# Performance work log

Measured on AMD Instinct MI355X. Metric: run time of the kernel, lower is better.

## Reference

```python
import jax, jax.numpy as jnp
import numpy as np

C_IN = 512
NUM_HEADS = 8
D_K = 64
D_V = 64


def setup_inputs() -> dict:
    key = jax.random.key(0)
    ks = jax.random.split(key, 6)
    scale = 1.0 / np.sqrt(C_IN)
    return {
        "x": jax.random.normal(ks[0], (8, C_IN, 32, 32), dtype=jnp.float32),
        "Wq": jax.random.normal(ks[1], (C_IN, NUM_HEADS * D_K), dtype=jnp.float32) * scale,
        "bq": jnp.zeros((NUM_HEADS * D_K,), dtype=jnp.float32),
        "Wk": jax.random.normal(ks[2], (C_IN, NUM_HEADS * D_K), dtype=jnp.float32) * scale,
        "bk": jnp.zeros((NUM_HEADS * D_K,), dtype=jnp.float32),
        "Wv": jax.random.normal(ks[3], (C_IN, NUM_HEADS * D_V), dtype=jnp.float32) * scale,
        "bv": jnp.zeros((NUM_HEADS * D_V,), dtype=jnp.float32),
        "Wo": jax.random.normal(ks[4], (NUM_HEADS * D_V, C_IN), dtype=jnp.float32) * scale,
        "bo": jnp.zeros((C_IN,), dtype=jnp.float32),
        "num_heads": NUM_HEADS,
    }


def reference(x, Wq, bq, Wk, bk, Wv, bv, Wo, bo, num_heads):
    B, C, H, W = x.shape
    S = H * W
    xs = x.reshape(B, C, S).transpose(0, 2, 1)  # [B, S, C]

    def split_heads(t):  # [B, S, nh*d] -> [B, nh, S, d]
        return t.reshape(B, S, num_heads, -1).transpose(0, 2, 1, 3)

    q = split_heads(xs @ Wq + bq)  # [B, nh, S, d_k]
    k = split_heads(xs @ Wk + bk)  # [B, nh, S, d_k]
    v = split_heads(xs @ Wv + bv)  # [B, nh, S, d_v]

    d_k = q.shape[-1]
    scores = jnp.einsum("bhqd,bhkd->bhqk", q, k) / jnp.sqrt(jnp.float32(d_k))
    probs = jax.nn.softmax(scores, axis=-1)
    attn = jnp.einsum("bhqk,bhkd->bhqd", probs, v)  # [B, nh, S, d_v]

    out = attn.transpose(0, 2, 1, 3).reshape(B, S, -1)  # [B, S, nh*d_v]
    out = out @ Wo + bo  # [B, S, C]
    out = out + xs  # residual
    return out.transpose(0, 2, 1).reshape(B, C, H, W)
```

## Files before the change

### kernel.cpp

```cpp
#include <hip/hip_runtime.h>

#define S_LEN 1024
#define CIN 512
#define NH 8
#define DH 64
#define NB 8

typedef short bf16x8 __attribute__((ext_vector_type(8)));
typedef float f32x4 __attribute__((ext_vector_type(4)));
typedef unsigned short u16x4 __attribute__((ext_vector_type(4)));

__device__ inline unsigned short f2bf(float f){
  union { float f; unsigned u; } v; v.f = f;
  unsigned r = v.u + 0x7FFFu + ((v.u >> 16) & 1u);
  return (unsigned short)(r >> 16);
}

__device__ inline void gload16(const void* g, void* l){
  __builtin_amdgcn_global_load_lds(
      (const __attribute__((address_space(1))) unsigned*)g,
      (__attribute__((address_space(3))) unsigned*)l, 16, 0, 0);
}

__device__ inline bf16x8 ldfrag(const unsigned short* lds, int row, int kbyte){
  return *(const bf16x8*)((const char*)lds + row*128 + (kbyte ^ ((row & 7) << 4)));
}

__global__ __launch_bounds__(256) void prep(const float* __restrict__ x,
    const float* __restrict__ Wq, const float* __restrict__ Wk,
    const float* __restrict__ Wv, const float* __restrict__ Wo,
    unsigned short* __restrict__ xs, unsigned short* __restrict__ Wqkt,
    unsigned short* __restrict__ Wvt, unsigned short* __restrict__ Wot){
  __shared__ unsigned short T[64*72];
  int bid = blockIdx.x, t = threadIdx.x;
  const float* src; unsigned short* dst; int ldS, r0, c0;
  if (bid < 1024){
    int b = bid >> 7, tt = bid & 127;
    src = x + (size_t)b*CIN*S_LEN; ldS = S_LEN;
    dst = xs + (size_t)b*S_LEN*CIN;
    r0 = (tt >> 4) * 64;
    c0 = (tt & 15) * 64;
  } else {
    int w = bid - 1024, mat = w >> 6, tt = w & 63;
    r0 = (tt >> 3) * 64; c0 = (tt & 7) * 64; ldS = 512;
    if (mat == 0){ src = Wq; dst = Wqkt; }
    else if (mat == 1){ src = Wk; dst = Wqkt + 512*512; }
    else if (mat == 2){ src = Wv; dst = Wvt; }
    else            { src = Wo; dst = Wot; }
  }
  int rl = t >> 4, cb = (t & 15) * 4;
  #pragma unroll
  for (int rr = 0; rr < 4; rr++){
    float4 f = *(const float4*)(src + (size_t)(r0 + rl + rr*16)*ldS + c0 + cb);
    int rc = rl + rr*16;
    T[(cb+0)*72 + rc] = f2bf(f.x);
    T[(cb+1)*72 + rc] = f2bf(f.y);
    T[(cb+2)*72 + rc] = f2bf(f.z);
    T[(cb+3)*72 + rc] = f2bf(f.w);
  }
  __syncthreads();
  int cl = t >> 2, rb = (t & 3) * 16;
  uint4 v0 = *(const uint4*)&T[cl*72 + rb];
  uint4 v1 = *(const uint4*)&T[cl*72 + rb + 8];
  *(uint4*)(dst + (size_t)(c0 + cl)*512 + r0 + rb) = v0;
  *(uint4*)(dst + (size_t)(c0 + cl)*512 + r0 + rb + 8) = v1;
}

__device__ inline void gemm128(const unsigned short* A, const unsigned short* B,
    unsigned short* As, unsigned short* Bs, f32x4 acc[4][4], int tid){
  int lane = tid & 63, w = tid >> 6;
  int wr = w >> 1, wc = w & 1;
  int srow = lane >> 3;
  int scol8 = ((lane & 7) ^ (lane >> 3)) << 3;
  for (int k0 = 0; k0 < 512; k0 += 64){
    __syncthreads();
    #pragma unroll
    for (int i = 0; i < 4; i++){
      int r0 = w*32 + i*8;
      gload16(A + (size_t)(r0 + srow)*512 + k0 + scol8, As + r0*64);
      gload16(B + (size_t)(r0 + srow)*512 + k0 + scol8, Bs + r0*64);
    }
    __syncthreads();
    #pragma unroll
    for (int kt = 0; kt < 2; kt++){
      bf16x8 af[4], bfv[4];
      #pragma unroll
      for (int i = 0; i < 4; i++){
        af[i]  = ldfrag(As, wr*64 + i*16 + (lane & 15), kt*64 + ((lane >> 4) << 4));
        bfv[i] = ldfrag(Bs, wc*64 + i*16 + (lane & 15), kt*64 + ((lane >> 4) << 4));
      }
      #pragma unroll
      for (int mi = 0; mi < 4; mi++)
        #pragma unroll
        for (int ni = 0; ni < 4; ni++)
          acc[mi][ni] = __builtin_amdgcn_mfma_f32_16x16x32_bf16(af[mi], bfv[ni], acc[mi][ni], 0,0,0);
    }
  }
}

__global__ __launch_bounds__(256) void qk128(const unsigned short* __restrict__ xs,
    const unsigned short* __restrict__ Wqkt, const float* __restrict__ bq,
    const float* __restrict__ bk, unsigned short* __restrict__ q_ws,
    unsigned short* __restrict__ k_ws){
  __shared__ __align__(16) unsigned short As[8192], Bs[8192];
  int tid = threadIdx.x, lane = tid & 63, w = tid >> 6, wr = w >> 1, wc = w & 1;
  int m0 = blockIdx.x * 128, n0 = blockIdx.y * 128, b = blockIdx.z;
  f32x4 acc[4][4];
  #pragma unroll
  for (int i = 0; i < 4; i++)
    #pragma unroll
    for (int j = 0; j < 4; j++) acc[i][j] = (f32x4){0.f,0.f,0.f,0.f};
  gemm128(xs + (size_t)b*S_LEN*CIN + (size_t)m0*512, Wqkt + (size_t)n0*512, As, Bs, acc, tid);
  int jb = (n0 + wc*64) >> 6;
  int isK = jb >= 8, h = jb & 7;
  const float* bias = isK ? bk : bq;
  unsigned short* dst = (isK ? k_ws : q_ws) + ((size_t)(b*NH + h))*S_LEN*DH;
  #pragma unroll
  for (int nt = 0; nt < 4; nt++){
    int d = nt*16 + (lane & 15);
    float bb = bias[(jb & 7)*64 + d];
    #pragma unroll
    for (int mi = 0; mi < 4; mi++)
      #pragma unroll
      for (int r = 0; r < 4; r++){
        int s = m0 + wr*64 + mi*16 + (lane >> 4)*4 + r;
        dst[(size_t)s*DH + d] = f2bf(acc[mi][nt][r] + bb);
      }
  }
}

__global__ __launch_bounds__(256) void vt128(const unsigned short* __restrict__ Wvt,
    const unsigned short* __restrict__ xs, const float* __restrict__ bv,
    unsigned short* __restrict__ vt_ws){
  __shared__ __align__(16) unsigned short As[8192], Bs[8192];
  int tid = threadIdx.x, lane = tid & 63, w = tid >> 6, wr = w >> 1, wc = w & 1;
  int m0 = blockIdx.x * 128, n0 = blockIdx.y * 128, b = blockIdx.z;
  f32x4 acc[4][4];
  #pragma unroll
  for (int i = 0; i < 4; i++)
    #pragma unroll
    for (int j = 0; j < 4; j++) acc[i][j] = (f32x4){0.f,0.f,0.f,0.f};
  gemm128(Wvt + (size_t)m0*512, xs + (size_t)b*S_LEN*CIN + (size_t)n0*512, As, Bs, acc, tid);
  #pragma unroll
  for (int mi = 0; mi < 4; mi++)
    #pragma unroll
    for (int r = 0; r < 4; r++){
      int j = m0 + wr*64 + mi*16 + (lane >> 4)*4 + r;
      int h = j >> 6, dv = j & 63;
      float bb = bv[j];
      unsigned short* dst = vt_ws + ((size_t)(b*NH + h)*DH + dv)*S_LEN;
      #pragma unroll
      for (int nt = 0; nt < 4; nt++){
        int s = n0 + wc*64 + nt*16 + (lane & 15);
        dst[s] = f2bf(acc[mi][nt][r] + bb);
      }
    }
}

__global__ __launch_bounds__(256) void attn_fwd(const unsigned short* __restrict__ qw,
    const unsigned short* __restrict__ kw, const unsigned short* __restrict__ vtw,
    unsigned short* __restrict__ aw){
  __shared__ __align__(16) unsigned short Ks[4096], Vs[4096], Ps[4096];
  int tid = threadIdx.x, lane = tid & 63, wid = tid >> 6;
  int bid = blockIdx.x;
  int idx = bid >> 3, qb = idx & 15, bh = (bid & 7)*8 + (idx >> 4);
  int qrw = lane & 15, g = lane >> 4;
  int q0 = qb*64 + wid*16;
  const unsigned short* qrow = qw + ((size_t)bh*S_LEN + q0 + qrw)*DH;
  bf16x8 qf0 = *(const bf16x8*)(qrow + g*8);
  bf16x8 qf1 = *(const bf16x8*)(qrow + 32 + g*8);
  unsigned short* myP = Ps + wid*1024;
  f32x4 oacc[4];
  #pragma unroll
  for (int i = 0; i < 4; i++) oacc[i] = (f32x4){0.f,0.f,0.f,0.f};
  float mrun = -1e30f, lrun = 0.f;

  for (int kv0 = 0; kv0 < S_LEN; kv0 += 64){
    __syncthreads();
    for (int i = tid; i < 512; i += 256){
      int row = i >> 3, ch = i & 7;
      *(uint4*)((char*)Ks + row*128 + ((ch*16) ^ ((row & 7) << 4))) =
          *(const uint4*)(kw + ((size_t)bh*S_LEN + kv0 + row)*DH + ch*8);
      *(uint4*)((char*)Vs + row*128 + ((ch*16) ^ ((row & 7) << 4))) =
          *(const uint4*)(vtw + ((size_t)bh*DH + row)*S_LEN + kv0 + ch*8);
    }
    __syncthreads();

    f32x4 st[4];
    #pragma unroll
    for (int mt = 0; mt < 4; mt++){
      f32x4 a = (f32x4){0.f,0.f,0.f,0.f};
      a = __builtin_amdgcn_mfma_f32_16x16x32_bf16(
            ldfrag(Ks, mt*16 + qrw, g << 4), qf0, a, 0,0,0);
      a = __builtin_amdgcn_mfma_f32_16x16x32_bf16(
            ldfrag(Ks, mt*16 + qrw, 64 + (g << 4)), qf1, a, 0,0,0);
      st[mt] = a;
    }
    float vmax = -1e30f;
    #pragma unroll
    for (int mt = 0; mt < 4; mt++)
      #pragma unroll
      for (int r = 0; r < 4; r++){
        st[mt][r] *= 0.125f;
        vmax = fmaxf(vmax, st[mt][r]);
      }
    vmax = fmaxf(vmax, __shfl_xor(vmax, 16));
    vmax = fmaxf(vmax, __shfl_xor(vmax, 32));
    float mnew = fmaxf(mrun, vmax);
    float corr = __expf(mrun - mnew);
    float psum = 0.f;
    #pragma unroll
    for (int mt = 0; mt < 4; mt++){
      float p0 = __expf(st[mt][0] - mnew);
      float p1 = __expf(st[mt][1] - mnew);
      float p2 = __expf(st[mt][2] - mnew);
      float p3 = __expf(st[mt][3] - mnew);
      psum += (p0 + p1) + (p2 + p3);
      u16x4 w; w[0]=f2bf(p0); w[1]=f2bf(p1); w[2]=f2bf(p2); w[3]=f2bf(p3);
      *(u16x4*)((char*)myP + qrw*128 + ((mt*32 + g*8) ^ ((qrw & 7) << 4))) = w;
    }
    psum += __shfl_xor(psum, 16);
    psum += __shfl_xor(psum, 32);
    lrun = lrun * corr + psum;
    mrun = mnew;
    #pragma unroll
    for (int mt = 0; mt < 4; mt++) oacc[mt] *= corr;
    #pragma unroll
    for (int kt = 0; kt < 2; kt++){
      bf16x8 pf = *(const bf16x8*)((char*)myP + qrw*128 +
                    ((kt*64 + (g << 4)) ^ ((qrw & 7) << 4)));
      #pragma unroll
      for (int mt = 0; mt < 4; mt++)
        oacc[mt] = __builtin_amdgcn_mfma_f32_16x16x32_bf16(
            ldfrag(Vs, mt*16 + qrw, kt*64 + (g << 4)), pf, oacc[mt], 0,0,0);
    }
  }
  float inv = 1.f / lrun;
  #pragma unroll
  for (int mt = 0; mt < 4; mt++)
    #pragma unroll
    for (int r = 0; r < 4; r++){
      int dv = mt*16 + g*4 + r;
      *(unsigned short*)((char*)myP + qrw*128 + ((dv*2) ^ ((qrw & 7) << 4))) =
          f2bf(oacc[mt][r] * inv);
    }
  int b = bh >> 3, h = bh & 7;
  int rr = lane >> 2, cc = lane & 3;
  uint4 lo = *(const uint4*)((char*)myP + rr*128 + ((cc*32) ^ ((rr & 7) << 4)));
  uint4 hi = *(const uint4*)((char*)myP + rr*128 + (((cc*32) + 16) ^ ((rr & 7) << 4)));
  unsigned short* obase = aw + ((size_t)b*S_LEN + (q0 + rr))*512 + h*64 + cc*16;
  *(uint4*)obase = lo;
  *(uint4*)(obase + 8) = hi;
}

__global__ __launch_bounds__(256) void out128(const unsigned short* __restrict__ Wot,
    const unsigned short* __restrict__ aw, const float* __restrict__ bo,
    const float* __restrict__ x, float* __restrict__ out){
  __shared__ __align__(16) unsigned short As[8192], Bs[8192];
  int tid = threadIdx.x, lane = tid & 63, w = tid >> 6, wr = w >> 1, wc = w & 1;
  int m0 = blockIdx.x * 128, n0 = blockIdx.y * 128, b = blockIdx.z;
  f32x4 acc[4][4];
  #pragma unroll
  for (int i = 0; i < 4; i++)
    #pragma unroll
    for (int j = 0; j < 4; j++) acc[i][j] = (f32x4){0.f,0.f,0.f,0.f};
  gemm128(Wot + (size_t)m0*512, aw + (size_t)b*S_LEN*512 + (size_t)n0*512, As, Bs, acc, tid);
  #pragma unroll
  for (int mi = 0; mi < 4; mi++)
    #pragma unroll
    for (int r = 0; r < 4; r++){
      int c = m0 + wr*64 + mi*16 + (lane >> 4)*4 + r;
      float bb = bo[c];
      size_t rowb = ((size_t)b*CIN + c)*S_LEN;
      #pragma unroll
      for (int nt = 0; nt < 4; nt++){
        int s = n0 + wc*64 + nt*16 + (lane & 15);
        out[rowb + s] = acc[mi][nt][r] + bb + x[rowb + s];
      }
    }
}

extern "C" void kernel_launch(void* const* d_in, const int* in_sizes, int n_in,
                              void* d_out, int out_size, void* d_ws, size_t ws_size,
                              hipStream_t stream){
  const float* x  = (const float*)d_in[0];
  const float* Wq = (const float*)d_in[1];
  const float* bq = (const float*)d_in[2];
  const float* Wk = (const float*)d_in[3];
  const float* bk = (const float*)d_in[4];
  const float* Wv = (const float*)d_in[5];
  const float* bv = (const float*)d_in[6];
  const float* Wo = (const float*)d_in[7];
  const float* bo = (const float*)d_in[8];
  float* out = (float*)d_out;

  unsigned short* p = (unsigned short*)d_ws;
  const size_t xs_e   = (size_t)NB*S_LEN*CIN;
  const size_t qkv_e  = (size_t)NB*NH*S_LEN*DH;
  unsigned short* xs    = p;                 p += xs_e;
  unsigned short* Wqkt  = p;                 p += 1024*512;
  unsigned short* Wvt   = p;                 p += 512*512;
  unsigned short* Wot   = p;                 p += 512*512;
  unsigned short* q_ws  = p;                 p += qkv_e;
  unsigned short* k_ws  = p;                 p += qkv_e;
  unsigned short* vt_ws = p;                 p += qkv_e;
  unsigned short* aw    = p;                 p += qkv_e;

  prep<<<1280, 256, 0, stream>>>(x, Wq, Wk, Wv, Wo, xs, Wqkt, Wvt, Wot);
  qk128<<<dim3(8, 8, NB), 256, 0, stream>>>(xs, Wqkt, bq, bk, q_ws, k_ws);
  vt128<<<dim3(4, 8, NB), 256, 0, stream>>>(Wvt, xs, bv, vt_ws);
  attn_fwd<<<1024, 256, 0, stream>>>(q_ws, k_ws, vt_ws, aw);
  out128<<<dim3(4, 8, NB), 256, 0, stream>>>(Wot, aw, bo, x, out);
}
```

Before: 168.6 us.

## Merge QK and V projection kernels; use direct-to-LDS loads and exp2 in attention

Folds the QK and V^T projection GEMMs into one launch with a 12-row grid: the first 8 rows compute Q/K tiles and the remaining 4 compute V^T tiles. This removes one kernel launch and lets both projections fill the GPU together. In attention, the K/V tile staging now uses global_load_lds with an XOR-swizzled source column instead of register round-trips. Softmax also switches to exp2 with log2(e) folded into the scale. The swizzle mapping must match ldfrag's layout, and exp2 changes rounding slightly.

```diff
diff --git a/kernel.cpp b/kernel.cpp
--- a/kernel.cpp
+++ b/kernel.cpp
@@ -98,63 +98,56 @@
   }
 }
 
-__global__ __launch_bounds__(256) void qk128(const unsigned short* __restrict__ xs,
-    const unsigned short* __restrict__ Wqkt, const float* __restrict__ bq,
-    const float* __restrict__ bk, unsigned short* __restrict__ q_ws,
-    unsigned short* __restrict__ k_ws){
+__global__ __launch_bounds__(256) void qkv128(const unsigned short* __restrict__ xs,
+    const unsigned short* __restrict__ Wqkt, const unsigned short* __restrict__ Wvt,
+    const float* __restrict__ bq, const float* __restrict__ bk,
+    const float* __restrict__ bv, unsigned short* __restrict__ q_ws,
+    unsigned short* __restrict__ k_ws, unsigned short* __restrict__ vt_ws){
   __shared__ __align__(16) unsigned short As[8192], Bs[8192];
   int tid = threadIdx.x, lane = tid & 63, w = tid >> 6, wr = w >> 1, wc = w & 1;
-  int m0 = blockIdx.x * 128, n0 = blockIdx.y * 128, b = blockIdx.z;
+  int bx = blockIdx.x, by = blockIdx.y, b = blockIdx.z;
   f32x4 acc[4][4];
   #pragma unroll
   for (int i = 0; i < 4; i++)
     #pragma unroll
     for (int j = 0; j < 4; j++) acc[i][j] = (f32x4){0.f,0.f,0.f,0.f};
-  gemm128(xs + (size_t)b*S_LEN*CIN + (size_t)m0*512, Wqkt + (size_t)n0*512, As, Bs, acc, tid);
-  int jb = (n0 + wc*64) >> 6;
-  int isK = jb >= 8, h = jb & 7;
-  const float* bias = isK ? bk : bq;
-  unsigned short* dst = (isK ? k_ws : q_ws) + ((size_t)(b*NH + h))*S_LEN*DH;
-  #pragma unroll
-  for (int nt = 0; nt < 4; nt++){
-    int d = nt*16 + (lane & 15);
-    float bb = bias[(jb & 7)*64 + d];
+  if (by < 8){
+    int m0 = bx * 128, n0 = by * 128;
+    gemm128(xs + (size_t)b*S_LEN*CIN + (size_t)m0*512, Wqkt + (size_t)n0*512, As, Bs, acc, tid);
+    int jb = (n0 + wc*64) >> 6;
+    int isK = jb >= 8, h = jb & 7;
+    const float* bias = isK ? bk : bq;
+    unsigned short* dst = (isK ? k_ws : q_ws) + ((size_t)(b*NH + h))*S_LEN*DH;
+    #pragma unroll
+    for (int nt = 0; nt < 4; nt++){
+      int d = nt*16 + (lane & 15);
+      float bb = bias[(jb & 7)*64 + d];
+      #pragma unroll
+      for (int mi = 0; mi < 4; mi++)
+        #pragma unroll
+        for (int r = 0; r < 4; r++){
+          int s = m0 + wr*64 + mi*16 + (lane >> 4)*4 + r;
+          dst[(size_t)s*DH + d] = f2bf(acc[mi][nt][r] + bb);
+        }
+    }
+  } else {
+    int m0 = (by - 8) * 128, n0 = bx * 128;
+    gemm128(Wvt + (size_t)m0*512, xs + (size_t)b*S_LEN*CIN + (size_t)n0*512, As, Bs, acc, tid);
     #pragma unroll
     for (int mi = 0; mi < 4; mi++)
       #pragma unroll
       for (int r = 0; r < 4; r++){
-        int s = m0 + wr*64 + mi*16 + (lane >> 4)*4 + r;
-        dst[(size_t)s*DH + d] = f2bf(acc[mi][nt][r] + bb);
+        int j = m0 + wr*64 + mi*16 + (lane >> 4)*4 + r;
+        int h = j >> 6, dv = j & 63;
+        float bb = bv[j];
+        unsigned short* dst = vt_ws + ((size_t)(b*NH + h)*DH + dv)*S_LEN;
+        #pragma unroll
+        for (int nt = 0; nt < 4; nt++){
+          int s = n0 + wc*64 + nt*16 + (lane & 15);
+          dst[s] = f2bf(acc[mi][nt][r] + bb);
+        }
       }
   }
-}
-
-__global__ __launch_bounds__(256) void vt128(const unsigned short* __restrict__ Wvt,
-    const unsigned short* __restrict__ xs, const float* __restrict__ bv,
-    unsigned short* __restrict__ vt_ws){
-  __shared__ __align__(16) unsigned short As[8192], Bs[8192];
-  int tid = threadIdx.x, lane = tid & 63, w = tid >> 6, wr = w >> 1, wc = w & 1;
-  int m0 = blockIdx.x * 128, n0 = blockIdx.y * 128, b = blockIdx.z;
-  f32x4 acc[4][4];
-  #pragma unroll
-  for (int i = 0; i < 4; i++)
-    #pragma unroll
-    for (int j = 0; j < 4; j++) acc[i][j] = (f32x4){0.f,0.f,0.f,0.f};
-  gemm128(Wvt + (size_t)m0*512, xs + (size_t)b*S_LEN*CIN + (size_t)n0*512, As, Bs, acc, tid);
-  #pragma unroll
-  for (int mi = 0; mi < 4; mi++)
-    #pragma unroll
-    for (int r = 0; r < 4; r++){
-      int j = m0 + wr*64 + mi*16 + (lane >> 4)*4 + r;
-      int h = j >> 6, dv = j & 63;
-      float bb = bv[j];
-      unsigned short* dst = vt_ws + ((size_t)(b*NH + h)*DH + dv)*S_LEN;
-      #pragma unroll
-      for (int nt = 0; nt < 4; nt++){
-        int s = n0 + wc*64 + nt*16 + (lane & 15);
-        dst[s] = f2bf(acc[mi][nt][r] + bb);
-      }
-    }
 }
 
 __global__ __launch_bounds__(256) void attn_fwd(const unsigned short* __restrict__ qw,
@@ -173,16 +166,19 @@
   f32x4 oacc[4];
   #pragma unroll
   for (int i = 0; i < 4; i++) oacc[i] = (f32x4){0.f,0.f,0.f,0.f};
-  float mrun = -1e30f, lrun = 0.f;
+  float mrun = -3e38f, lrun = 0.f;
+  int srow = lane >> 3, scol8 = ((lane & 7) ^ (lane >> 3)) << 3;
+  const unsigned short* kbase = kw + (size_t)bh*S_LEN*DH;
+  const unsigned short* vbase = vtw + (size_t)bh*DH*S_LEN;
+  const float SC = 0.125f * 1.44269504f;
 
   for (int kv0 = 0; kv0 < S_LEN; kv0 += 64){
     __syncthreads();
-    for (int i = tid; i < 512; i += 256){
-      int row = i >> 3, ch = i & 7;
-      *(uint4*)((char*)Ks + row*128 + ((ch*16) ^ ((row & 7) << 4))) =
-          *(const uint4*)(kw + ((size_t)bh*S_LEN + kv0 + row)*DH + ch*8);
-      *(uint4*)((char*)Vs + row*128 + ((ch*16) ^ ((row & 7) << 4))) =
-          *(const uint4*)(vtw + ((size_t)bh*DH + row)*S_LEN + kv0 + ch*8);
+    #pragma unroll
+    for (int i = 0; i < 2; i++){
+      int r0 = wid*16 + i*8;
+      gload16(kbase + (size_t)(kv0 + r0 + srow)*DH + scol8, Ks + r0*64);
+      gload16(vbase + (size_t)(r0 + srow)*S_LEN + kv0 + scol8, Vs + r0*64);
     }
     __syncthreads();
 
@@ -196,25 +192,25 @@
             ldfrag(Ks, mt*16 + qrw, 64 + (g << 4)), qf1, a, 0,0,0);
       st[mt] = a;
     }
-    float vmax = -1e30f;
+    float vmax = -3e38f;
     #pragma unroll
     for (int mt = 0; mt < 4; mt++)
       #pragma unroll
       for (int r = 0; r < 4; r++){
-        st[mt][r] *= 0.125f;
+        st[mt][r] *= SC;
         vmax = fmaxf(vmax, st[mt][r]);
       }
     vmax = fmaxf(vmax, __shfl_xor(vmax, 16));
     vmax = fmaxf(vmax, __shfl_xor(vmax, 32));
     float mnew = fmaxf(mrun, vmax);
-    float corr = __expf(mrun - mnew);
+    float corr = __builtin_amdgcn_exp2f(mrun - mnew);
     float psum = 0.f;
     #pragma unroll
     for (int mt = 0; mt < 4; mt++){
-      float p0 = __expf(st[mt][0] - mnew);
-      float p1 = __expf(st[mt][1] - mnew);
-      float p2 = __expf(st[mt][2] - mnew);
-      float p3 = __expf(st[mt][3] - mnew);
+      float p0 = __builtin_amdgcn_exp2f(st[mt][0] - mnew);
+      float p1 = __builtin_amdgcn_exp2f(st[mt][1] - mnew);
+      float p2 = __builtin_amdgcn_exp2f(st[mt][2] - mnew);
+      float p3 = __builtin_amdgcn_exp2f(st[mt][3] - mnew);
       psum += (p0 + p1) + (p2 + p3);
       u16x4 w; w[0]=f2bf(p0); w[1]=f2bf(p1); w[2]=f2bf(p2); w[3]=f2bf(p3);
       *(u16x4*)((char*)myP + qrw*128 + ((mt*32 + g*8) ^ ((qrw & 7) << 4))) = w;
@@ -307,8 +303,7 @@
   unsigned short* aw    = p;                 p += qkv_e;
 
   prep<<<1280, 256, 0, stream>>>(x, Wq, Wk, Wv, Wo, xs, Wqkt, Wvt, Wot);
-  qk128<<<dim3(8, 8, NB), 256, 0, stream>>>(xs, Wqkt, bq, bk, q_ws, k_ws);
-  vt128<<<dim3(4, 8, NB), 256, 0, stream>>>(Wvt, xs, bv, vt_ws);
+  qkv128<<<dim3(8, 12, NB), 256, 0, stream>>>(xs, Wqkt, Wvt, bq, bk, bv, q_ws, k_ws, vt_ws);
   attn_fwd<<<1024, 256, 0, stream>>>(q_ws, k_ws, vt_ws, aw);
   out128<<<dim3(4, 8, NB), 256, 0, stream>>>(Wot, aw, bo, x, out);
 }
```

New measurement: 163.4 us. -3.1%, faster.
